# Optimization experiments

Hardware: AMD Instinct MI355X
Metric: run time of the kernel (lower is better)

Reference implementation:

```python
import jax, jax.numpy as jnp
import numpy as np

EPS = 1e-5
DEPTH = 6
HEADS = 8
DIM_HEAD = 64

def layer_norm(x, g, b):
    m = jnp.mean(x, axis=-1, keepdims=True)
    v = jnp.mean((x - m) ** 2, axis=-1, keepdims=True)
    return (x - m) * jax.lax.rsqrt(v + EPS) * g + b

def setup_inputs() -> dict:
    key = jax.random.key(0)
    ks = jax.random.split(key, 12)
    b, T, F, v, D = 4, 8, 16, 196, 768
    L, inner, ffh = DEPTH, HEADS * DIM_HEAD, 4 * D
    s = 0.02
    return {
        "x": jax.random.normal(ks[0], (b, T, F, v, D), jnp.float32),
        "latents": jax.random.normal(ks[1], (64, D), jnp.float32),
        "frame_emb": jax.random.normal(ks[2], (F, D), jnp.float32),
        "time_emb": jax.random.normal(ks[3], (T, 1, D), jnp.float32),
        "ln_m_g": jnp.ones((L, D), jnp.float32),
        "ln_m_b": jnp.zeros((L, D), jnp.float32),
        "ln_l_g": jnp.ones((L, D), jnp.float32),
        "ln_l_b": jnp.zeros((L, D), jnp.float32),
        "Wq": jax.random.normal(ks[4], (L, D, inner), jnp.float32) * s,
        "Wk": jax.random.normal(ks[5], (L, D, inner), jnp.float32) * s,
        "Wv": jax.random.normal(ks[6], (L, D, inner), jnp.float32) * s,
        "Wo": jax.random.normal(ks[7], (L, inner, D), jnp.float32) * s,
        "ff_ln_g": jnp.ones((L, D), jnp.float32),
        "ff_ln_b": jnp.zeros((L, D), jnp.float32),
        "W1": jax.random.normal(ks[8], (L, D, ffh), jnp.float32) * s,
        "W2": jax.random.normal(ks[9], (L, ffh, D), jnp.float32) * s,
        "out_ln_g": jnp.ones((D,), jnp.float32),
        "out_ln_b": jnp.zeros((D,), jnp.float32),
    }

def perceiver_attention(x, lat, g_m, b_m, g_l, b_l, Wq, Wk, Wv, Wo):
    # x: [b, Nx, D], lat: [b, Nz, D]
    b, Nz, D = lat.shape
    xm = layer_norm(x, g_m, b_m)
    ln = layer_norm(lat, g_l, b_l)
    q = (ln @ Wq).reshape(b, Nz, HEADS, DIM_HEAD).transpose(0, 2, 1, 3)  # b h q d
    kv = jnp.concatenate([xm, ln], axis=1)  # b (Nx+Nz) D
    Nf = kv.shape[1]
    k = (kv @ Wk).reshape(b, Nf, HEADS, DIM_HEAD).transpose(0, 2, 1, 3)
    v = (kv @ Wv).reshape(b, Nf, HEADS, DIM_HEAD).transpose(0, 2, 1, 3)
    q = q * (DIM_HEAD ** -0.5)
    sim = jnp.einsum('bhqd,bhfd->bhqf', q, k)
    alphas = jax.nn.softmax(sim, axis=-1)
    out = jnp.einsum('bhqf,bhfd->bhqd', alphas, v)
    out = out.transpose(0, 2, 1, 3).reshape(b, Nz, HEADS * DIM_HEAD)
    return out @ Wo

def reference(x, latents, frame_emb, time_emb, ln_m_g, ln_m_b, ln_l_g, ln_l_b,
              Wq, Wk, Wv, Wo, ff_ln_g, ff_ln_b, W1, W2, out_ln_g, out_ln_b):
    b, T, F, v, D = x.shape
    x = x + frame_emb[:F][None, None, :, None, :]           # frame embeddings
    x = x.reshape(b, T, F * v, D)
    x = x + time_emb[:T][None]                              # time pos embeddings (broadcast over n)
    x = x.reshape(b, T * F * v, D)
    lat = jnp.broadcast_to(latents[None], (b,) + latents.shape)
    for i in range(DEPTH):
        lat = lat + perceiver_attention(x, lat, ln_m_g[i], ln_m_b[i], ln_l_g[i], ln_l_b[i],
                                        Wq[i], Wk[i], Wv[i], Wo[i])
        h = layer_norm(lat, ff_ln_g[i], ff_ln_b[i])
        lat = lat + jax.nn.gelu(h @ W1[i], approximate=False) @ W2[i]
    return layer_norm(lat, out_ln_g, out_ln_b)
```

## Files before the change

kernel.cpp:

```cpp
#include <hip/hip_runtime.h>
#include <cstdint>
#include <cstddef>

typedef unsigned short u16;
typedef __attribute__((ext_vector_type(8))) short short8;
typedef __attribute__((ext_vector_type(4))) float f4;

#define LNEPS 1e-5f

__device__ __forceinline__ float b2f(u16 u){
  union { unsigned u; float f; } x; x.u = ((unsigned)u) << 16; return x.f;
}
__device__ __forceinline__ u16 f2b(float f){
  union { float f; unsigned u; } x; x.f = f;
  unsigned r = x.u + 0x7fffu + ((x.u >> 16) & 1u);
  return (u16)(r >> 16);
}
__device__ __forceinline__ float ldin(const void* p, long i, int f){
  return f ? ((const float*)p)[i] : b2f(((const u16*)p)[i]);
}

__global__ void detect_k(const u16* __restrict__ g1, int* __restrict__ flag) {
  int isf32 = 1, isbf = 1;
  for (int i = 0; i < 8; i++) {
    if (g1[2 * i] != 0 || g1[2 * i + 1] != 0x3F80) isf32 = 0;
    if (g1[i] != 0x3F80) isbf = 0;
  }
  *flag = (isf32 && !isbf) ? 1 : 0;
}

__global__ void cvt_k(const void* __restrict__ in, u16* __restrict__ out, long n,
                      const int* __restrict__ flag) {
  int f = *flag;
  for (long i = (long)blockIdx.x * 256 + threadIdx.x; i < n; i += (long)gridDim.x * 256)
    out[i] = f ? f2b(((const float*)in)[i]) : ((const u16*)in)[i];
}

__global__ __launch_bounds__(256) void transpose_in(const void* __restrict__ in,
                                                    u16* __restrict__ out,
                                                    int R, int C, long inZ, long outZ,
                                                    const int* __restrict__ flag) {
  __shared__ u16 tile[32][33];
  int f = *flag;
  long ib = (long)blockIdx.z * inZ;
  u16* op = out + (long)blockIdx.z * outZ;
  int c0 = blockIdx.x * 32, r0 = blockIdx.y * 32;
  int tx = threadIdx.x & 31, ty = threadIdx.x >> 5;
  #pragma unroll
  for (int k = 0; k < 4; k++) {
    int ry = ty + 8 * k;
    long idx = ib + (long)(r0 + ry) * C + c0 + tx;
    tile[ry][tx] = f ? f2b(((const float*)in)[idx]) : ((const u16*)in)[idx];
  }
  __syncthreads();
  #pragma unroll
  for (int k = 0; k < 4; k++) {
    int cy = ty + 8 * k;
    op[(long)(c0 + cy) * R + r0 + tx] = tile[tx][cy];
  }
}

__global__ __launch_bounds__(256) void transpose_b16(const u16* __restrict__ in,
                                                     u16* __restrict__ out,
                                                     int R, int C, long inZ, long outZ) {
  __shared__ u16 tile[32][33];
  const u16* ip = in + (long)blockIdx.z * inZ;
  u16* op = out + (long)blockIdx.z * outZ;
  int c0 = blockIdx.x * 32, r0 = blockIdx.y * 32;
  int tx = threadIdx.x & 31, ty = threadIdx.x >> 5;
  #pragma unroll
  for (int k = 0; k < 4; k++) {
    int ry = ty + 8 * k;
    tile[ry][tx] = ip[(long)(r0 + ry) * C + c0 + tx];
  }
  __syncthreads();
  #pragma unroll
  for (int k = 0; k < 4; k++) {
    int cy = ty + 8 * k;
    op[(long)(c0 + cy) * R + r0 + tx] = tile[tx][cy];
  }
}

__global__ __launch_bounds__(256) void compute_xn_k(const void* __restrict__ x,
                                                    const void* __restrict__ fe,
                                                    const void* __restrict__ te,
                                                    u16* __restrict__ xn,
                                                    const int* __restrict__ flag) {
  int f = *flag;
  long r = blockIdx.x;
  int rem = (int)(r % 25088);
  int tt = rem / 3136;
  int fi = (rem % 3136) / 196;
  int t = threadIdx.x;
  float vals[3]; float s = 0.f, s2 = 0.f;
  #pragma unroll
  for (int i = 0; i < 3; i++) {
    int c = t + 256 * i;
    float v = ldin(x, r * 768 + c, f) + ldin(fe, (long)fi * 768 + c, f)
            + ldin(te, (long)tt * 768 + c, f);
    vals[i] = v; s += v; s2 += v * v;
  }
  __shared__ float red[8];
  #pragma unroll
  for (int m = 32; m; m >>= 1) { s += __shfl_xor(s, m); s2 += __shfl_xor(s2, m); }
  int w = t >> 6;
  if ((t & 63) == 0) { red[w] = s; red[4 + w] = s2; }
  __syncthreads();
  float S = red[0] + red[1] + red[2] + red[3];
  float S2 = red[4] + red[5] + red[6] + red[7];
  float mean = S * (1.f / 768.f);
  float var = S2 * (1.f / 768.f) - mean * mean;
  float inv = rsqrtf(var + LNEPS);
  #pragma unroll
  for (int i = 0; i < 3; i++) {
    int c = t + 256 * i;
    xn[r * 768 + c] = f2b((vals[i] - mean) * inv);
  }
}

__global__ __launch_bounds__(256) void ln_rows_k(const float* __restrict__ src,
                                                 const u16* __restrict__ g,
                                                 const u16* __restrict__ bb,
                                                 void* __restrict__ dst,
                                                 const int* __restrict__ flag,
                                                 int outSel) {
  int of32 = outSel ? *flag : 0;
  long r = blockIdx.x;
  const float* xr = src + r * 768;
  int t = threadIdx.x;
  float vals[3]; float s = 0.f, s2 = 0.f;
  #pragma unroll
  for (int i = 0; i < 3; i++) {
    float v = xr[t + 256 * i]; vals[i] = v; s += v; s2 += v * v;
  }
  __shared__ float red[8];
  #pragma unroll
  for (int m = 32; m; m >>= 1) { s += __shfl_xor(s, m); s2 += __shfl_xor(s2, m); }
  int w = t >> 6;
  if ((t & 63) == 0) { red[w] = s; red[4 + w] = s2; }
  __syncthreads();
  float S = red[0] + red[1] + red[2] + red[3];
  float S2 = red[4] + red[5] + red[6] + red[7];
  float mean = S * (1.f / 768.f);
  float var = S2 * (1.f / 768.f) - mean * mean;
  float inv = rsqrtf(var + LNEPS);
  #pragma unroll
  for (int i = 0; i < 3; i++) {
    int c = t + 256 * i;
    float v = (vals[i] - mean) * inv * b2f(g[c]) + b2f(bb[c]);
    if (of32) ((float*)dst)[r * 768 + c] = v;
    else      ((u16*)dst)[r * 768 + c] = f2b(v);
  }
}

__global__ void init_lat_k(const void* __restrict__ latents, float* __restrict__ lat,
                           const int* __restrict__ flag) {
  int f = *flag;
  long i = (long)blockIdx.x * 256 + threadIdx.x;
  lat[i] = ldin(latents, i % 49152, f);
}

__global__ void zero_f32_k(float* __restrict__ p, long n) {
  for (long i = (long)blockIdx.x * 256 + threadIdx.x; i < n; i += (long)gridDim.x * 256)
    p[i] = 0.f;
}

__global__ void report_k(u16* out, float v) { out[0] = f2b(v); }

__global__ __launch_bounds__(256) void bias_proj_k(const u16* __restrict__ bm,
                                                   const u16* __restrict__ WkT,
                                                   const u16* __restrict__ WvT,
                                                   float* __restrict__ bk,
                                                   float* __restrict__ bv) {
  int t = blockIdx.x * 256 + threadIdx.x;
  int j = t & 511;
  const u16* row = ((t >> 9) ? WvT : WkT) + (long)j * 768;
  float s = 0.f;
  for (int d = 0; d < 768; d++) s += b2f(bm[d]) * b2f(row[d]);
  ((t >> 9) ? bv : bk)[j] = s;
}

__global__ __launch_bounds__(256) void prep_small_k(const u16* __restrict__ qkv,
                                                    const float* __restrict__ bk,
                                                    float* __restrict__ s_lat,
                                                    float* __restrict__ latmax,
                                                    float* __restrict__ cbias) {
  int t = threadIdx.x; int wv = t >> 6, lane = t & 63;
  int r = blockIdx.x * 4 + wv;
  int b = r >> 9, hq = r & 511, h = hq >> 6, qi = hq & 63;
  const u16* qrow = qkv + ((long)(b * 64 + qi)) * 1536 + h * 64;
  const u16* krow = qkv + ((long)(b * 64 + lane)) * 1536 + 512 + h * 64;
  float s = 0.f;
  for (int d = 0; d < 64; d++) s += b2f(qrow[d]) * b2f(krow[d]);
  s *= 0.125f;
  s_lat[(long)r * 64 + lane] = s;
  float cb = b2f(qrow[lane]) * bk[h * 64 + lane];
  float mx = s;
  #pragma unroll
  for (int m = 32; m; m >>= 1) { mx = fmaxf(mx, __shfl_xor(mx, m)); cb += __shfl_xor(cb, m); }
  if (lane == 0) { latmax[r] = mx; cbias[r] = 0.125f * cb; }
}

__global__ __launch_bounds__(256) void softmax_rows_k(u16* __restrict__ St,
                                                      const float* __restrict__ latmax,
                                                      const float* __restrict__ s_lat,
                                                      float* __restrict__ mrow,
                                                      float* __restrict__ sxrow,
                                                      float* __restrict__ linv) {
  const int NCH = 3136;
  long r = blockIdx.x;
  uint4* row4 = (uint4*)(St + r * 25088L);
  int t = threadIdx.x; int lane = t & 63, w = t >> 6;
  __shared__ float red[8];
  float mx = -3e38f;
  for (int c = t; c < NCH; c += 256) {
    uint4 u = row4[c];
    mx = fmaxf(mx, b2f((u16)(u.x & 0xffff))); mx = fmaxf(mx, b2f((u16)(u.x >> 16)));
    mx = fmaxf(mx, b2f((u16)(u.y & 0xffff))); mx = fmaxf(mx, b2f((u16)(u.y >> 16)));
    mx = fmaxf(mx, b2f((u16)(u.z & 0xffff))); mx = fmaxf(mx, b2f((u16)(u.z >> 16)));
    mx = fmaxf(mx, b2f((u16)(u.w & 0xffff))); mx = fmaxf(mx, b2f((u16)(u.w >> 16)));
  }
  #pragma unroll
  for (int m = 32; m; m >>= 1) mx = fmaxf(mx, __shfl_xor(mx, m));
  if (lane == 0) red[w] = mx;
  __syncthreads();
  float mv = fmaxf(fmaxf(red[0], red[1]), fmaxf(red[2], red[3]));
  mv = fmaxf(mv, latmax[r]);
  __syncthreads();
  if (w == 0) {
    float e = expf(s_lat[r * 64 + lane] - mv);
    #pragma unroll
    for (int m = 32; m; m >>= 1) e += __shfl_xor(e, m);
    if (lane == 0) red[4] = e;
  }
  float sum = 0.f;
  for (int c = t; c < NCH; c += 256) {
    uint4 u = row4[c];
    float e0 = expf(b2f((u16)(u.x & 0xffff)) - mv), e1 = expf(b2f((u16)(u.x >> 16)) - mv);
    float e2 = expf(b2f((u16)(u.y & 0xffff)) - mv), e3 = expf(b2f((u16)(u.y >> 16)) - mv);
    float e4 = expf(b2f((u16)(u.z & 0xffff)) - mv), e5 = expf(b2f((u16)(u.z >> 16)) - mv);
    float e6 = expf(b2f((u16)(u.w & 0xffff)) - mv), e7 = expf(b2f((u16)(u.w >> 16)) - mv);
    sum += ((e0 + e1) + (e2 + e3)) + ((e4 + e5) + (e6 + e7));
    u.x = (unsigned)f2b(e0) | ((unsigned)f2b(e1) << 16);
    u.y = (unsigned)f2b(e2) | ((unsigned)f2b(e3) << 16);
    u.z = (unsigned)f2b(e4) | ((unsigned)f2b(e5) << 16);
    u.w = (unsigned)f2b(e6) | ((unsigned)f2b(e7) << 16);
    row4[c] = u;
  }
  #pragma unroll
  for (int m = 32; m; m >>= 1) sum += __shfl_xor(sum, m);
  if (lane == 0) red[w] = sum;
  __syncthreads();
  if (t == 0) {
    float sx = red[0] + red[1] + red[2] + red[3];
    mrow[r] = mv; sxrow[r] = sx;
    linv[r] = 1.0f / (sx + red[4]);
  }
}

__global__ void ctxg_k(const float* __restrict__ CTX, const u16* __restrict__ gm,
                       u16* __restrict__ CTXg, long n) {
  for (long i = (long)blockIdx.x * 256 + threadIdx.x; i < n; i += (long)gridDim.x * 256) {
    int c = (int)(i % 768);
    CTXg[i] = f2b(CTX[i] * b2f(gm[c]));
  }
}

__global__ __launch_bounds__(256) void out_lat_k(const u16* __restrict__ qkv,
                                                 const float* __restrict__ s_lat,
                                                 const float* __restrict__ mrow,
                                                 float* __restrict__ out_lat) {
  int t = threadIdx.x; int wv = t >> 6, lane = t & 63;
  int r = blockIdx.x * 4 + wv;
  int b = r >> 9, hq = r & 511, h = hq >> 6;
  float mv = mrow[r];
  const u16* vbase = qkv + ((long)(b * 64)) * 1536 + 1024 + h * 64 + lane;
  float a = 0.f;
  for (int fl = 0; fl < 64; fl++)
    a += expf(s_lat[(long)r * 64 + fl] - mv) * b2f(vbase[(long)fl * 1536]);
  out_lat[(long)r * 64 + lane] = a;
}

struct GemmP {
  const u16* A; const u16* B; void* C;
  long lda, ldb, ldc;
  int M, N, K, kPerSplit, mtiles, numH;
  long aSB, aSH, bSB, bSH, cSB, cSH;
  float scale;
  const float* rowBias;
  const u16* colScaleB;
  const float* sxv; const float* colBiasF; const float* addMat; const float* rowScale;
};

__device__ __forceinline__ void glds16(const u16* g, u16* l) {
  __builtin_amdgcn_global_load_lds((const __attribute__((address_space(1))) void*)g,
                                   (__attribute__((address_space(3))) void*)l, 16, 0, 0);
}

template <int EPI>
__device__ __forceinline__ void epi_store(const GemmP& p, int zb, int zh,
                                          float v, int row, int col) {
  u16* Cb = (u16*)p.C + (long)zb * p.cSB + (long)zh * p.cSH;
  float* Cf = (float*)p.C + (long)zb * p.cSB + (long)zh * p.cSH;
  if constexpr (EPI == 0) {
    Cb[(long)row * p.ldc + col] = f2b(v);
  } else if constexpr (EPI == 2) {
    atomicAdd(&Cf[(long)row * p.ldc + col], v);
  } else if constexpr (EPI == 3) {
    v += p.rowBias[(long)zb * p.M + row];
    Cb[(long)row * p.ldc + col] = f2b(v);
  } else if constexpr (EPI == 4) {
    float g = 0.5f * v * (1.0f + erff(v * 0.70710678118f));
    Cb[(long)row * p.ldc + col] = f2b(g);
  } else if constexpr (EPI == 5) {
    long rb = (long)zb * 512 + zh * 64 + row;
    v = (v + p.sxv[rb] * p.colBiasF[zh * 64 + col] + p.addMat[rb * 64 + col]) * p.rowScale[rb];
    Cb[(long)row * p.ldc + col] = f2b(v);
  } else if constexpr (EPI == 6) {
    v *= b2f(p.colScaleB[col]);
    Cb[(long)row * p.ldc + col] = f2b(v);
  }
}

template <int EPI>
__global__ __launch_bounds__(256, 2) void gemm_bt(GemmP p) {
  __shared__ u16 As[2][4096];
  __shared__ u16 Bs[2][4096];
  const int t = threadIdx.x;

  const int gx = gridDim.x, gy = gridDim.y, gz = gridDim.z;
  const int splits = gy / p.mtiles;
  const long total = (long)gx * gy * gz;
  const long fid = blockIdx.x + (long)gx * ((long)blockIdx.y + (long)gy * blockIdx.z);
  const long qq = total >> 3, rr = total & 7;
  const long xcd = fid & 7, idx = fid >> 3;
  const long logical = (xcd < rr ? xcd * (qq + 1) : rr * (qq + 1) + (xcd - rr) * qq) + idx;
  const int mt = (int)(logical % p.mtiles);
  const long l1 = logical / p.mtiles;
  const int bxn = (int)(l1 % gx);
  const long l2 = l1 / gx;
  const int split = (int)(l2 % splits);
  const int z = (int)(l2 / splits);

  const int zb = z / p.numH, zh = z - zb * p.numH;
  const u16* A = p.A + (long)zb * p.aSB + (long)zh * p.aSH;
  const u16* B = p.B + (long)zb * p.bSB + (long)zh * p.bSH;
  const int tm = mt * 128, tn = bxn * 128;
  const int K0 = split * p.kPerSplit;
  const int Kend = min(p.K, K0 + p.kPerSplit);

  const int c0 = t, c1 = t + 256;
  const int ko0 = c0 >> 7, mm0 = c0 & 127;
  const int ko1 = c1 >> 7, mm1 = c1 & 127;
  const int ra0 = min(tm + mm0, p.M - 1);
  const int ra1 = min(tm + mm1, p.M - 1);
  const int rb0 = min(tn + mm0, p.N - 1);
  const int rb1 = min(tn + mm1, p.N - 1);
  const u16* pa0 = A + (long)ra0 * p.lda + ko0 * 8;
  const u16* pa1 = A + (long)ra1 * p.lda + ko1 * 8;
  const u16* pb0 = B + (long)rb0 * p.ldb + ko0 * 8;
  const u16* pb1 = B + (long)rb1 * p.ldb + ko1 * 8;

  const int lane = t & 63, w = t >> 6;
  const int wm = w >> 1, wn = w & 1;
  const int lm = lane & 15, lg = lane >> 4;
  const int lOffA = (lg * 128 + wm * 64 + lm) * 8;
  const int lOffB = (lg * 128 + wn * 64 + lm) * 8;

  f4 acc[4][4];
  #pragma unroll
  for (int i = 0; i < 4; i++)
    #pragma unroll
    for (int j = 0; j < 4; j++) acc[i][j] = f4{0.f, 0.f, 0.f, 0.f};

  glds16(pa0 + K0, &As[0][c0 * 8]);
  glds16(pa1 + K0, &As[0][c1 * 8]);
  glds16(pb0 + K0, &Bs[0][c0 * 8]);
  glds16(pb1 + K0, &Bs[0][c1 * 8]);
  __syncthreads();

  int cur = 0;
  for (int kk = K0; kk < Kend; kk += 32) {
    const int nxt = kk + 32;
    if (nxt < Kend) {
      glds16(pa0 + nxt, &As[cur ^ 1][c0 * 8]);
      glds16(pa1 + nxt, &As[cur ^ 1][c1 * 8]);
      glds16(pb0 + nxt, &Bs[cur ^ 1][c0 * 8]);
      glds16(pb1 + nxt, &Bs[cur ^ 1][c1 * 8]);
    }
    const u16* lA = &As[cur][lOffA];
    const u16* lB = &Bs[cur][lOffB];
    short8 av[4], bvf[4];
    #pragma unroll
    for (int i = 0; i < 4; i++) av[i] = *(const short8*)(lA + i * 128);
    #pragma unroll
    for (int j = 0; j < 4; j++) bvf[j] = *(const short8*)(lB + j * 128);
    #pragma unroll
    for (int i = 0; i < 4; i++)
      #pragma unroll
      for (int j = 0; j < 4; j++)
        acc[i][j] = __builtin_amdgcn_mfma_f32_16x16x32_bf16(av[i], bvf[j], acc[i][j], 0, 0, 0);
    __syncthreads();
    cur ^= 1;
  }

  #pragma unroll
  for (int i = 0; i < 4; i++) {
    #pragma unroll
    for (int j = 0; j < 4; j++) {
      int col = tn + wn * 64 + j * 16 + lm;
      int row0 = tm + wm * 64 + i * 16 + lg * 4;
      #pragma unroll
      for (int rr2 = 0; rr2 < 4; rr2++) {
        int row = row0 + rr2;
        if (row < p.M && col < p.N)
          epi_store<EPI>(p, zb, zh, acc[i][j][rr2] * p.scale, row, col);
      }
    }
  }
}

template <int EPI>
__global__ __launch_bounds__(512, 2) void gemm_bt8(GemmP p) {
  __shared__ u16 As[4][8192];
  __shared__ u16 Bs[4][8192];
  const int t = threadIdx.x;

  const int gx = gridDim.x, gy = gridDim.y, gz = gridDim.z;
  const int splits = gy / p.mtiles;
  const long total = (long)gx * gy * gz;
  const long fid = blockIdx.x + (long)gx * ((long)blockIdx.y + (long)gy * blockIdx.z);
  const long qq = total >> 3, rr = total & 7;
  const long xcd = fid & 7, idx = fid >> 3;
  const long logical = (xcd < rr ? xcd * (qq + 1) : rr * (qq + 1) + (xcd - rr) * qq) + idx;
  const int mt = (int)(logical % p.mtiles);
  const long l1 = logical / p.mtiles;
  const int bxn = (int)(l1 % gx);
  const long l2 = l1 / gx;
  const int split = (int)(l2 % splits);
  const int z = (int)(l2 / splits);

  const int zb = z / p.numH, zh = z - zb * p.numH;
  const u16* A = p.A + (long)zb * p.aSB + (long)zh * p.aSH;
  const u16* B = p.B + (long)zb * p.bSB + (long)zh * p.bSH;
  const int tm = mt * 256, tn = bxn * 256;
  const int K0 = split * p.kPerSplit;
  const int nkt = (min(p.K, K0 + p.kPerSplit) - K0) >> 5;

  const int r0 = t & 255, kc0 = t >> 8;
  const int raA = min(tm + r0, p.M - 1);
  const int rbB = min(tn + r0, p.N - 1);
  const u16* paL0 = A + (long)raA * p.lda + K0 + kc0 * 8;
  const u16* paL1 = A + (long)raA * p.lda + K0 + (2 + kc0) * 8;
  const u16* pbL0 = B + (long)rbB * p.ldb + K0 + kc0 * 8;
  const u16* pbL1 = B + (long)rbB * p.ldb + K0 + (2 + kc0) * 8;

  const int lane = t & 63, w = t >> 6;
  const int wm = w >> 2, wn = w & 3;
  const int lm = lane & 15, lg = lane >> 4;
  const int aBase = lg * 2048 + (wm * 128 + lm) * 8;
  const int bBase = lg * 2048 + (wn * 64 + lm) * 8;

  f4 acc[8][4];
  #pragma unroll
  for (int i = 0; i < 8; i++)
    #pragma unroll
    for (int j = 0; j < 4; j++) acc[i][j] = f4{0.f, 0.f, 0.f, 0.f};

  {
    glds16(paL0, &As[0][t * 8]);
    glds16(paL1, &As[0][4096 + t * 8]);
    glds16(pbL0, &Bs[0][t * 8]);
    glds16(pbL1, &Bs[0][4096 + t * 8]);
    glds16(paL0 + 32, &As[1][t * 8]);
    glds16(paL1 + 32, &As[1][4096 + t * 8]);
    glds16(pbL0 + 32, &Bs[1][t * 8]);
    glds16(pbL1 + 32, &Bs[1][4096 + t * 8]);
  }

  for (int kt = 0; kt < nkt; ++kt) {
    if (kt + 1 < nkt) asm volatile("s_waitcnt vmcnt(4)" ::: "memory");
    else              asm volatile("s_waitcnt vmcnt(0)" ::: "memory");
    __builtin_amdgcn_s_barrier();
    asm volatile("" ::: "memory");

    const int s = kt & 3;
    const u16* sa = &As[s][aBase];
    const u16* sb = &Bs[s][bBase];
    const long ko = (long)(kt + 2) * 32;
    const int s2 = (kt + 2) & 3;

    if (kt + 2 < nkt) {
      glds16(paL0 + ko, &As[s2][t * 8]);
      glds16(paL1 + ko, &As[s2][4096 + t * 8]);
    }
    short8 bv4[4];
    #pragma unroll
    for (int j = 0; j < 4; j++) bv4[j] = *(const short8*)(sb + j * 128);
    {
      short8 av[4];
      #pragma unroll
      for (int i = 0; i < 4; i++) av[i] = *(const short8*)(sa + i * 128);
      __builtin_amdgcn_s_setprio(1);
      #pragma unroll
      for (int i = 0; i < 4; i++)
        #pragma unroll
        for (int j = 0; j < 4; j++)
          acc[i][j] = __builtin_amdgcn_mfma_f32_16x16x32_bf16(av[i], bv4[j], acc[i][j], 0, 0, 0);
      __builtin_amdgcn_s_setprio(0);
    }
    if (kt + 2 < nkt) {
      glds16(pbL0 + ko, &Bs[s2][t * 8]);
      glds16(pbL1 + ko, &Bs[s2][4096 + t * 8]);
    }
    {
      short8 av[4];
      #pragma unroll
      for (int i = 0; i < 4; i++) av[i] = *(const short8*)(sa + (4 + i) * 128);
      __builtin_amdgcn_s_setprio(1);
      #pragma unroll
      for (int i = 0; i < 4; i++)
        #pragma unroll
        for (int j = 0; j < 4; j++)
          acc[4 + i][j] = __builtin_amdgcn_mfma_f32_16x16x32_bf16(av[i], bv4[j], acc[4 + i][j], 0, 0, 0);
      __builtin_amdgcn_s_setprio(0);
    }
    asm volatile("" ::: "memory");
  }

  #pragma unroll
  for (int i = 0; i < 8; i++) {
    #pragma unroll
    for (int j = 0; j < 4; j++) {
      int col = tn + wn * 64 + j * 16 + lm;
      int row0 = tm + wm * 128 + i * 16 + lg * 4;
      #pragma unroll
      for (int rr2 = 0; rr2 < 4; rr2++) {
        int row = row0 + rr2;
        if (row < p.M && col < p.N)
          epi_store<EPI>(p, zb, zh, acc[i][j][rr2] * p.scale, row, col);
      }
    }
  }
}

static inline void gemm_launch(int epi, dim3 g, const GemmP& p, hipStream_t s) {
  switch (epi) {
    case 0: gemm_bt<0><<<g, 256, 0, s>>>(p); break;
    case 2: gemm_bt<2><<<g, 256, 0, s>>>(p); break;
    case 3: gemm_bt<3><<<g, 256, 0, s>>>(p); break;
    case 4: gemm_bt<4><<<g, 256, 0, s>>>(p); break;
    case 5: gemm_bt<5><<<g, 256, 0, s>>>(p); break;
    case 6: gemm_bt<6><<<g, 256, 0, s>>>(p); break;
  }
}

static inline void gemm_launch8(int epi, dim3 g, const GemmP& p, hipStream_t s) {
  switch (epi) {
    case 2: gemm_bt8<2><<<g, 512, 0, s>>>(p); break;
    case 3: gemm_bt8<3><<<g, 512, 0, s>>>(p); break;
  }
}

extern "C" void kernel_launch(void* const* d_in, const int* in_sizes, int n_in,
                              void* d_out, int out_size, void* d_ws, size_t ws_size,
                              hipStream_t stream) {
  (void)in_sizes; (void)n_in; (void)out_size;
  const void* x      = d_in[0];
  const void* lats   = d_in[1];
  const void* frame  = d_in[2];
  const void* timee  = d_in[3];
  const void* ln_m_g = d_in[4];
  const void* ln_m_b = d_in[5];
  const void* ln_l_g = d_in[6];
  const void* ln_l_b = d_in[7];
  const void* Wq     = d_in[8];
  const void* Wk     = d_in[9];
  const void* Wv     = d_in[10];
  const void* Wo     = d_in[11];
  const void* ff_g   = d_in[12];
  const void* ff_b   = d_in[13];
  const void* W1     = d_in[14];
  const void* W2     = d_in[15];
  const void* og     = d_in[16];
  const void* ob     = d_in[17];

  char* ws = (char*)d_ws;
  size_t off = 0;
  auto alloc = [&](size_t bytes) -> char* {
    char* p = ws + off;
    off = (off + bytes + 255) & ~(size_t)255;
    return p;
  };
  int*   flag  = (int*)alloc(4);
  u16*   Xn    = (u16*)alloc(77070336ULL * 2);
  u16*   XnT   = (u16*)alloc(77070336ULL * 2);
  u16*   St    = (u16*)alloc(51380224ULL * 2);
  u16*   WT3   = (u16*)alloc(7077888ULL * 2);
  u16*   WoT   = (u16*)alloc(2359296ULL * 2);
  u16*   W1T   = (u16*)alloc(14155776ULL * 2);
  u16*   W2T   = (u16*)alloc(14155776ULL * 2);
  u16*   WkC   = (u16*)alloc(2359296ULL * 2);
  u16*   pMg   = (u16*)alloc(4608ULL * 2);
  u16*   pMb   = (u16*)alloc(4608ULL * 2);
  u16*   pLg   = (u16*)alloc(4608ULL * 2);
  u16*   pLb   = (u16*)alloc(4608ULL * 2);
  u16*   pFg   = (u16*)alloc(4608ULL * 2);
  u16*   pFb   = (u16*)alloc(4608ULL * 2);
  u16*   pOg   = (u16*)alloc(768ULL * 2);
  u16*   pOb   = (u16*)alloc(768ULL * 2);
  float* lat   = (float*)alloc(196608ULL * 4);
  u16*   lnb   = (u16*)alloc(196608ULL * 2);
  u16*   qkv   = (u16*)alloc(393216ULL * 2);
  u16*   QT    = (u16*)alloc(1572864ULL * 2);
  float* s_lat = (float*)alloc(131072ULL * 4);
  float* bk    = (float*)alloc(512 * 4);
  float* bvv   = (float*)alloc(512 * 4);
  float* cbias = (float*)alloc(2048 * 4);
  float* latmx = (float*)alloc(2048 * 4);
  float* mrow  = (float*)alloc(2048 * 4);
  float* sxrow = (float*)alloc(2048 * 4);
  float* linv  = (float*)alloc(2048 * 4);
  float* CTX   = (float*)alloc(1572864ULL * 4);
  u16*   CTXg  = (u16*)alloc(1572864ULL * 2);
  float* outl  = (float*)alloc(131072ULL * 4);
  u16*   ao    = (u16*)alloc(131072ULL * 2);
  u16*   hbuf  = (u16*)alloc(196608ULL * 2);
  u16*   t1g   = (u16*)alloc(786432ULL * 2);

  if (off > ws_size) {
    report_k<<<1, 1, 0, stream>>>((u16*)d_out, (float)ws_size);
    return;
  }

  detect_k<<<1, 1, 0, stream>>>((const u16*)ln_m_g, flag);
  cvt_k<<<18, 256, 0, stream>>>(ln_m_g, pMg, 4608, flag);
  cvt_k<<<18, 256, 0, stream>>>(ln_m_b, pMb, 4608, flag);
  cvt_k<<<18, 256, 0, stream>>>(ln_l_g, pLg, 4608, flag);
  cvt_k<<<18, 256, 0, stream>>>(ln_l_b, pLb, 4608, flag);
  cvt_k<<<18, 256, 0, stream>>>(ff_g, pFg, 4608, flag);
  cvt_k<<<18, 256, 0, stream>>>(ff_b, pFb, 4608, flag);
  cvt_k<<<3, 256, 0, stream>>>(og, pOg, 768, flag);
  cvt_k<<<3, 256, 0, stream>>>(ob, pOb, 768, flag);
  cvt_k<<<2048, 256, 0, stream>>>(Wk, WkC, 2359296, flag);

  transpose_in<<<dim3(16, 24, 6), 256, 0, stream>>>(Wq, WT3 + 0 * 393216, 768, 512, 393216, 1179648, flag);
  transpose_in<<<dim3(16, 24, 6), 256, 0, stream>>>(Wk, WT3 + 1 * 393216, 768, 512, 393216, 1179648, flag);
  transpose_in<<<dim3(16, 24, 6), 256, 0, stream>>>(Wv, WT3 + 2 * 393216, 768, 512, 393216, 1179648, flag);
  transpose_in<<<dim3(24, 16, 6), 256, 0, stream>>>(Wo, WoT, 512, 768, 393216, 393216, flag);
  transpose_in<<<dim3(96, 24, 6), 256, 0, stream>>>(W1, W1T, 768, 3072, 2359296, 2359296, flag);
  transpose_in<<<dim3(24, 96, 6), 256, 0, stream>>>(W2, W2T, 3072, 768, 2359296, 2359296, flag);
  compute_xn_k<<<100352, 256, 0, stream>>>(x, frame, timee, Xn, flag);
  transpose_b16<<<dim3(24, 784, 4), 256, 0, stream>>>(Xn, XnT, 25088, 768, 19267584, 19267584);
  init_lat_k<<<768, 256, 0, stream>>>(lats, lat, flag);

  for (int l = 0; l < 6; l++) {
    const u16* WkC_l = WkC + (long)l * 393216;
    const u16* WT3_l = WT3 + (long)l * 1179648;

    ln_rows_k<<<256, 256, 0, stream>>>(lat, pLg + l * 768, pLb + l * 768, lnb, flag, 0);

    {
      GemmP p{}; p.A = lnb; p.B = WT3_l; p.C = qkv;
      p.lda = 768; p.ldb = 768; p.ldc = 1536;
      p.M = 256; p.N = 1536; p.K = 768; p.kPerSplit = 768; p.mtiles = 2; p.numH = 1;
      p.scale = 1.f;
      gemm_launch(0, dim3(12, 2, 1), p, stream);
    }
    {
      GemmP p{}; p.A = qkv; p.B = WkC_l; p.C = QT;
      p.lda = 1536; p.ldb = 512; p.ldc = 768;
      p.M = 64; p.N = 768; p.K = 64; p.kPerSplit = 64; p.mtiles = 1; p.numH = 8;
      p.aSB = 98304; p.aSH = 64; p.bSB = 0; p.bSH = 64; p.cSB = 393216; p.cSH = 49152;
      p.scale = 0.125f; p.colScaleB = pMg + l * 768;
      gemm_launch(6, dim3(6, 1, 32), p, stream);
    }
    bias_proj_k<<<4, 256, 0, stream>>>(pMb + l * 768, WT3_l + 393216, WT3_l + 786432, bk, bvv);
    prep_small_k<<<512, 256, 0, stream>>>(qkv, bk, s_lat, latmx, cbias);
    zero_f32_k<<<1536, 256, 0, stream>>>(CTX, 1572864);

    {
      GemmP p{}; p.A = QT; p.B = Xn; p.C = St;
      p.lda = 768; p.ldb = 768; p.ldc = 25088;
      p.M = 512; p.N = 25088; p.K = 768; p.kPerSplit = 768; p.mtiles = 2; p.numH = 1;
      p.aSB = 393216; p.bSB = 19267584; p.cSB = 12845056;
      p.scale = 1.f; p.rowBias = cbias;
      gemm_launch8(3, dim3(98, 2, 4), p, stream);
    }
    softmax_rows_k<<<2048, 256, 0, stream>>>(St, latmx, s_lat, mrow, sxrow, linv);

    {
      GemmP p{}; p.A = St; p.B = XnT; p.C = CTX;
      p.lda = 25088; p.ldb = 25088; p.ldc = 768;
      p.M = 512; p.N = 768; p.K = 25088; p.kPerSplit = 896; p.mtiles = 2; p.numH = 1;
      p.aSB = 12845056; p.bSB = 19267584; p.cSB = 393216;
      p.scale = 1.f;
      gemm_launch8(2, dim3(3, 56, 4), p, stream);
    }
    ctxg_k<<<1536, 256, 0, stream>>>(CTX, pMg + l * 768, CTXg, 1572864);
    out_lat_k<<<512, 256, 0, stream>>>(qkv, s_lat, mrow, outl);

    {
      GemmP p{}; p.A = CTXg; p.B = WT3_l + 2 * 393216; p.C = ao;
      p.lda = 768; p.ldb = 768; p.ldc = 512;
      p.M = 64; p.N = 64; p.K = 768; p.kPerSplit = 768; p.mtiles = 1; p.numH = 8;
      p.aSB = 393216; p.aSH = 49152; p.bSB = 0; p.bSH = 49152; p.cSB = 32768; p.cSH = 64;
      p.scale = 1.f; p.sxv = sxrow; p.colBiasF = bvv; p.addMat = outl; p.rowScale = linv;
      gemm_launch(5, dim3(1, 1, 32), p, stream);
    }
    {
      GemmP p{}; p.A = ao; p.B = WoT + (long)l * 393216; p.C = lat;
      p.lda = 512; p.ldb = 512; p.ldc = 768;
      p.M = 256; p.N = 768; p.K = 512; p.kPerSplit = 512; p.mtiles = 2; p.numH = 1;
      p.scale = 1.f;
      gemm_launch(2, dim3(6, 2, 1), p, stream);
    }
    ln_rows_k<<<256, 256, 0, stream>>>(lat, pFg + l * 768, pFb + l * 768, hbuf, flag, 0);
    {
      GemmP p{}; p.A = hbuf; p.B = W1T + (long)l * 2359296; p.C = t1g;
      p.lda = 768; p.ldb = 768; p.ldc = 3072;
      p.M = 256; p.N = 3072; p.K = 768; p.kPerSplit = 768; p.mtiles = 2; p.numH = 1;
      p.scale = 1.f;
      gemm_launch(4, dim3(24, 2, 1), p, stream);
    }
    {
      GemmP p{}; p.A = t1g; p.B = W2T + (long)l * 2359296; p.C = lat;
      p.lda = 3072; p.ldb = 3072; p.ldc = 768;
      p.M = 256; p.N = 768; p.K = 3072; p.kPerSplit = 768; p.mtiles = 2; p.numH = 1;
      p.scale = 1.f;
      gemm_launch(2, dim3(6, 8, 1), p, stream);
    }
  }
  ln_rows_k<<<256, 256, 0, stream>>>(lat, pOg, pOb, d_out, flag, 1);
}
```

Before: 5.113 ms.

## Swizzle LDS layout and deepen prefetch pipeline in 256x256 GEMM; reduce split-K

Rewrites the 512-thread GEMM so each thread loads four 8-element chunks per row (row-major 32-wide tiles) with an XOR swizzle. The swizzle is meant to avoid LDS bank conflicts on MFMA operand reads. The prefetch depth goes from 2 to 3 stages in flight within the same 4-buffer ring. The split-K for the attention-times-V GEMM drops from 28 to 8 splits, which cuts atomic accumulation traffic but leaves fewer blocks to fill the GPU.

```diff
diff --git a/kernel.cpp b/kernel.cpp
--- a/kernel.cpp
+++ b/kernel.cpp
@@ -421,7 +421,7 @@
 }
 
 template <int EPI>
-__global__ __launch_bounds__(512, 2) void gemm_bt8(GemmP p) {
+__global__ __launch_bounds__(512, 2) void gemm8p(GemmP p) {
   __shared__ u16 As[4][8192];
   __shared__ u16 Bs[4][8192];
   const int t = threadIdx.x;
@@ -445,21 +445,38 @@
   const u16* B = p.B + (long)zb * p.bSB + (long)zh * p.bSH;
   const int tm = mt * 256, tn = bxn * 256;
   const int K0 = split * p.kPerSplit;
-  const int nkt = (min(p.K, K0 + p.kPerSplit) - K0) >> 5;
-
-  const int r0 = t & 255, kc0 = t >> 8;
-  const int raA = min(tm + r0, p.M - 1);
-  const int rbB = min(tn + r0, p.N - 1);
-  const u16* paL0 = A + (long)raA * p.lda + K0 + kc0 * 8;
-  const u16* paL1 = A + (long)raA * p.lda + K0 + (2 + kc0) * 8;
-  const u16* pbL0 = B + (long)rbB * p.ldb + K0 + kc0 * 8;
-  const u16* pbL1 = B + (long)rbB * p.ldb + K0 + (2 + kc0) * 8;
+  const int nk = (min(p.K, K0 + p.kPerSplit) - K0) >> 5;
+
+  const int rloc = t >> 2, uu = t & 3;
+  const int swz0 = (rloc ^ (rloc >> 2)) & 3;
+  const int rloc1 = 128 + rloc;
+  const int swz1 = (rloc1 ^ (rloc1 >> 2)) & 3;
+  const int gA0 = min(tm + rloc,  p.M - 1), gA1 = min(tm + rloc1, p.M - 1);
+  const int gB0 = min(tn + rloc,  p.N - 1), gB1 = min(tn + rloc1, p.N - 1);
+  const u16* pa0 = A + (long)gA0 * p.lda + K0 + (uu ^ swz0) * 8;
+  const u16* pa1 = A + (long)gA1 * p.lda + K0 + (uu ^ swz1) * 8;
+  const u16* pb0 = B + (long)gB0 * p.ldb + K0 + (uu ^ swz0) * 8;
+  const u16* pb1 = B + (long)gB1 * p.ldb + K0 + (uu ^ swz1) * 8;
+
+#define STAGE_A(s) { u16* d = (u16*)As[(s) & 3]; long ko = (long)(s) * 32; \
+    glds16(pa0 + ko, d + t * 8); glds16(pa1 + ko, d + 4096 + t * 8); }
+#define STAGE_B(s) { u16* d = (u16*)Bs[(s) & 3]; long ko = (long)(s) * 32; \
+    glds16(pb0 + ko, d + t * 8); glds16(pb1 + ko, d + 4096 + t * 8); }
 
   const int lane = t & 63, w = t >> 6;
   const int wm = w >> 2, wn = w & 3;
   const int lm = lane & 15, lg = lane >> 4;
-  const int aBase = lg * 2048 + (wm * 128 + lm) * 8;
-  const int bBase = lg * 2048 + (wn * 64 + lm) * 8;
+  int aIdx[8], bIdx[4];
+  #pragma unroll
+  for (int i = 0; i < 8; i++) {
+    int r = wm * 128 + i * 16 + lm;
+    aIdx[i] = r * 32 + ((lg ^ ((r ^ (r >> 2)) & 3)) * 8);
+  }
+  #pragma unroll
+  for (int j = 0; j < 4; j++) {
+    int r = wn * 64 + j * 16 + lm;
+    bIdx[j] = r * 32 + ((lg ^ ((r ^ (r >> 2)) & 3)) * 8);
+  }
 
   f4 acc[8][4];
   #pragma unroll
@@ -467,66 +484,45 @@
     #pragma unroll
     for (int j = 0; j < 4; j++) acc[i][j] = f4{0.f, 0.f, 0.f, 0.f};
 
-  {
-    glds16(paL0, &As[0][t * 8]);
-    glds16(paL1, &As[0][4096 + t * 8]);
-    glds16(pbL0, &Bs[0][t * 8]);
-    glds16(pbL1, &Bs[0][4096 + t * 8]);
-    glds16(paL0 + 32, &As[1][t * 8]);
-    glds16(paL1 + 32, &As[1][4096 + t * 8]);
-    glds16(pbL0 + 32, &Bs[1][t * 8]);
-    glds16(pbL1 + 32, &Bs[1][4096 + t * 8]);
-  }
-
-  for (int kt = 0; kt < nkt; ++kt) {
-    if (kt + 1 < nkt) asm volatile("s_waitcnt vmcnt(4)" ::: "memory");
-    else              asm volatile("s_waitcnt vmcnt(0)" ::: "memory");
-    __builtin_amdgcn_s_barrier();
-    asm volatile("" ::: "memory");
-
-    const int s = kt & 3;
-    const u16* sa = &As[s][aBase];
-    const u16* sb = &Bs[s][bBase];
-    const long ko = (long)(kt + 2) * 32;
-    const int s2 = (kt + 2) & 3;
-
-    if (kt + 2 < nkt) {
-      glds16(paL0 + ko, &As[s2][t * 8]);
-      glds16(paL1 + ko, &As[s2][4096 + t * 8]);
-    }
-    short8 bv4[4];
-    #pragma unroll
-    for (int j = 0; j < 4; j++) bv4[j] = *(const short8*)(sb + j * 128);
-    {
-      short8 av[4];
+  STAGE_A(0); STAGE_B(0);
+  STAGE_A(1); STAGE_B(1);
+  STAGE_A(2); STAGE_B(2);
+
+  for (int s = 0; s < nk; ++s) {
+    const int rem = nk - 1 - s;
+    if (rem >= 2)      asm volatile("s_waitcnt vmcnt(8)" ::: "memory");
+    else if (rem == 1) asm volatile("s_waitcnt vmcnt(4)" ::: "memory");
+    else               asm volatile("s_waitcnt vmcnt(0)" ::: "memory");
+    asm volatile("s_barrier" ::: "memory");
+
+    const u16* sa = As[s & 3];
+    const u16* sb = Bs[s & 3];
+    short8 bv[4], av[4], av2[4];
+    #pragma unroll
+    for (int j = 0; j < 4; j++) bv[j] = *(const short8*)(sb + bIdx[j]);
+    #pragma unroll
+    for (int i = 0; i < 4; i++) av[i] = *(const short8*)(sa + aIdx[i]);
+    if (s + 3 < nk) STAGE_A(s + 3);
+    __builtin_amdgcn_s_setprio(1);
+    #pragma unroll
+    for (int i = 0; i < 4; i++)
       #pragma unroll
-      for (int i = 0; i < 4; i++) av[i] = *(const short8*)(sa + i * 128);
-      __builtin_amdgcn_s_setprio(1);
+      for (int j = 0; j < 4; j++)
+        acc[i][j] = __builtin_amdgcn_mfma_f32_16x16x32_bf16(av[i], bv[j], acc[i][j], 0, 0, 0);
+    __builtin_amdgcn_s_setprio(0);
+    #pragma unroll
+    for (int i = 0; i < 4; i++) av2[i] = *(const short8*)(sa + aIdx[4 + i]);
+    if (s + 3 < nk) STAGE_B(s + 3);
+    __builtin_amdgcn_s_setprio(1);
+    #pragma unroll
+    for (int i = 0; i < 4; i++)
       #pragma unroll
-      for (int i = 0; i < 4; i++)
-        #pragma unroll
-        for (int j = 0; j < 4; j++)
-          acc[i][j] = __builtin_amdgcn_mfma_f32_16x16x32_bf16(av[i], bv4[j], acc[i][j], 0, 0, 0);
-      __builtin_amdgcn_s_setprio(0);
-    }
-    if (kt + 2 < nkt) {
-      glds16(pbL0 + ko, &Bs[s2][t * 8]);
-      glds16(pbL1 + ko, &Bs[s2][4096 + t * 8]);
-    }
-    {
-      short8 av[4];
-      #pragma unroll
-      for (int i = 0; i < 4; i++) av[i] = *(const short8*)(sa + (4 + i) * 128);
-      __builtin_amdgcn_s_setprio(1);
-      #pragma unroll
-      for (int i = 0; i < 4; i++)
-        #pragma unroll
-        for (int j = 0; j < 4; j++)
-          acc[4 + i][j] = __builtin_amdgcn_mfma_f32_16x16x32_bf16(av[i], bv4[j], acc[4 + i][j], 0, 0, 0);
-      __builtin_amdgcn_s_setprio(0);
-    }
-    asm volatile("" ::: "memory");
-  }
+      for (int j = 0; j < 4; j++)
+        acc[4 + i][j] = __builtin_amdgcn_mfma_f32_16x16x32_bf16(av2[i], bv[j], acc[4 + i][j], 0, 0, 0);
+    __builtin_amdgcn_s_setprio(0);
+  }
+#undef STAGE_A
+#undef STAGE_B
 
   #pragma unroll
   for (int i = 0; i < 8; i++) {
@@ -557,8 +553,8 @@
 
 static inline void gemm_launch8(int epi, dim3 g, const GemmP& p, hipStream_t s) {
   switch (epi) {
-    case 2: gemm_bt8<2><<<g, 512, 0, s>>>(p); break;
-    case 3: gemm_bt8<3><<<g, 512, 0, s>>>(p); break;
+    case 2: gemm8p<2><<<g, 512, 0, s>>>(p); break;
+    case 3: gemm8p<3><<<g, 512, 0, s>>>(p); break;
   }
 }
 
@@ -692,10 +688,10 @@
     {
       GemmP p{}; p.A = St; p.B = XnT; p.C = CTX;
       p.lda = 25088; p.ldb = 25088; p.ldc = 768;
-      p.M = 512; p.N = 768; p.K = 25088; p.kPerSplit = 896; p.mtiles = 2; p.numH = 1;
+      p.M = 512; p.N = 768; p.K = 25088; p.kPerSplit = 3136; p.mtiles = 2; p.numH = 1;
       p.aSB = 12845056; p.bSB = 19267584; p.cSB = 393216;
       p.scale = 1.f;
-      gemm_launch8(2, dim3(3, 56, 4), p, stream);
+      gemm_launch8(2, dim3(3, 16, 4), p, stream);
     }
     ctxg_k<<<1536, 256, 0, stream>>>(CTX, pMg + l * 768, CTXg, 1572864);
     out_lat_k<<<512, 256, 0, stream>>>(qkv, s_lat, mrow, outl);
```

Result: faster. 4.591 ms (-10.2%).
